# Kernel optimization log

Measured on AMD Instinct MI355X. Metric: run time of the kernel, lower is better.

The kernel has to match this reference:

```python
import jax, jax.numpy as jnp
import numpy as np
from jax import lax

KSIZE = 3
SIGMA = 0.3 * ((KSIZE - 1) * 0.5 - 1) + 0.8  # cv2 auto-sigma for k=3 -> 0.8

def _gauss_kernel(k, sigma):
    ax = np.arange(k, dtype=np.float64) - (k - 1) / 2
    xx, yy = np.meshgrid(ax, ax, indexing='ij')
    ker = np.exp(-(xx ** 2 + yy ** 2) / (2.0 * sigma ** 2))
    ker /= ker.sum()
    return jnp.asarray(ker, jnp.float32)

SCHARR_X = jnp.array([[-3., 0., 3.], [-10., 0., 10.], [-3., 0., 3.]], jnp.float32)
SCHARR_Y = SCHARR_X.T  # cv2.Scharr(dy=1)

def _conv2d_reflect(img, ker):
    # img: [B,1,H,W]; cross-correlation (like cv2.filter2D) with BORDER_REFLECT_101
    p = ker.shape[0] // 2
    img = jnp.pad(img, ((0, 0), (0, 0), (p, p), (p, p)), mode='reflect')
    return lax.conv_general_dilated(img, ker[None, None], (1, 1), 'VALID')

def setup_inputs() -> dict:
    key = jax.random.key(0)
    x = jax.random.uniform(key, (8, 3, 1024, 1024), dtype=jnp.float32) * 255.0
    return {"x": x}

def reference(x):
    B, C, H, W = x.shape
    # cv2 RGB2GRAY weights
    rgb_w = jnp.array([0.299, 0.587, 0.114], dtype=x.dtype)
    gray = jnp.einsum('bchw,c->bhw', x, rgb_w)[:, None]  # [B,1,H,W]
    blurred = _conv2d_reflect(gray, _gauss_kernel(KSIZE, SIGMA))
    sx = _conv2d_reflect(blurred, SCHARR_X)
    sy = _conv2d_reflect(blurred, SCHARR_Y)
    mag = jnp.sqrt(sx * sx + sy * sy)  # L2_gradient=True
    # forward returns gradient magnitude replicated across channels
    return jnp.broadcast_to(mag, (B, C, H, W))
```

## Files before the change

kernel.cpp:

```cpp
#include <hip/hip_runtime.h>
#include <math.h>


#define IMG_H 1024
#define IMG_W 1024
#define TH 32
#define TW 128
#define GYR (TH + 4)
#define GXD 136
#define NIT ((GYR * (GXD/4) + 255) / 256)
#define NITEMS (GYR * (GXD/4))

#define W0 0.52201125f
#define W1 0.23899437f
#define AV0 0.71698311f
#define AV1 3.95597745f
#define AV2 6.65407872f

__device__ __forceinline__ int reflect101(int v, int n) {
    v = (v < 0) ? -v : v;
    return (v >= n) ? (2 * n - 2 - v) : v;
}

__global__ __launch_bounds__(256)
void edge_kernel(const float* __restrict__ in, float* __restrict__ out, int B) {
    __shared__ float sg[GYR][GXD];

    const int tid = threadIdx.x;
    const int x0 = blockIdx.x * TW;
    const int y0 = blockIdx.y * TH;
    const int b  = blockIdx.z;

    const size_t plane = (size_t)IMG_H * IMG_W;
    const float* pr = in + (size_t)b * 3 * plane;
    const float* pg = pr + plane;
    const float* pb = pg + plane;

    float4 R[NIT], G[NIT], Bv[NIT];
    #pragma unroll
    for (int it = 0; it < NIT; ++it) {
        int i = tid + it * 256;
        if (i < NITEMS) {
            int gy  = i / (GXD / 4);
            int gx4 = (i - gy * (GXD / 4)) * 4;
            int y = reflect101(y0 - 2 + gy, IMG_H);
            int x = x0 - 4 + gx4;
            if ((unsigned)x <= (unsigned)(IMG_W - 4)) {
                size_t o = (size_t)y * IMG_W + x;
                R[it]  = *(const float4*)(pr + o);
                G[it]  = *(const float4*)(pg + o);
                Bv[it] = *(const float4*)(pb + o);
            } else {
                int xe0 = reflect101(x,     IMG_W), xe1 = reflect101(x + 1, IMG_W);
                int xe2 = reflect101(x + 2, IMG_W), xe3 = reflect101(x + 3, IMG_W);
                size_t ro = (size_t)y * IMG_W;
                R[it]  = make_float4(pr[ro+xe0], pr[ro+xe1], pr[ro+xe2], pr[ro+xe3]);
                G[it]  = make_float4(pg[ro+xe0], pg[ro+xe1], pg[ro+xe2], pg[ro+xe3]);
                Bv[it] = make_float4(pb[ro+xe0], pb[ro+xe1], pb[ro+xe2], pb[ro+xe3]);
            }
        }
    }
    #pragma unroll
    for (int it = 0; it < NIT; ++it) {
        int i = tid + it * 256;
        if (i < NITEMS) {
            int gy  = i / (GXD / 4);
            int gx4 = (i - gy * (GXD / 4)) * 4;
            float4 gr;
            gr.x = 0.299f * R[it].x + 0.587f * G[it].x + 0.114f * Bv[it].x;
            gr.y = 0.299f * R[it].y + 0.587f * G[it].y + 0.114f * Bv[it].y;
            gr.z = 0.299f * R[it].z + 0.587f * G[it].z + 0.114f * Bv[it].z;
            gr.w = 0.299f * R[it].w + 0.587f * G[it].w + 0.114f * Bv[it].w;
            *(float4*)&sg[gy][gx4] = gr;
        }
    }
    __syncthreads();

    const int tx  = tid & 31;
    const int tyg = tid >> 5;
    const int c4  = tx * 4;
    const int r0  = tyg * 4;

    float hs[5][4], hd[5][4];

    auto hrow = [&](int rr, float* HS, float* HD) {
        const float* row = &sg[rr][c4];
        float4 ga = *(const float4*)(row);
        float4 gb = *(const float4*)(row + 4);
        float4 gc = *(const float4*)(row + 8);
        float g[12] = {ga.x, ga.y, ga.z, ga.w, gb.x, gb.y, gb.z, gb.w,
                       gc.x, gc.y, gc.z, gc.w};
        #pragma unroll
        for (int k = 0; k < 4; ++k) {
            HS[k] = AV0 * (g[k+2] + g[k+6]) + AV1 * (g[k+3] + g[k+5]) + AV2 * g[k+4];
            HD[k] = W1 * (g[k+6] - g[k+2]) + W0 * (g[k+5] - g[k+3]);
        }
    };

    #pragma unroll
    for (int s = 0; s < 5; ++s) hrow(r0 + s, hs[s], hd[s]);

    float* po = out + (size_t)b * 3 * plane;
    #pragma unroll
    for (int t = 0; t < 4; ++t) {
        if (t > 0) hrow(r0 + 4 + t, hs[(t + 4) % 5], hd[(t + 4) % 5]);
        const int i0 = t % 5, i1 = (t+1) % 5, i2 = (t+2) % 5, i3 = (t+3) % 5, i4 = (t+4) % 5;
        float4 mag;
        float* mp = &mag.x;
        #pragma unroll
        for (int k = 0; k < 4; ++k) {
            float sx = AV0 * (hd[i0][k] + hd[i4][k]) + AV1 * (hd[i1][k] + hd[i3][k]) + AV2 * hd[i2][k];
            float sy = W1 * (hs[i4][k] - hs[i0][k]) + W0 * (hs[i3][k] - hs[i1][k]);
            mp[k] = sqrtf(sx * sx + sy * sy);
        }
        size_t o = (size_t)(y0 + r0 + t) * IMG_W + (x0 + c4);
        *(float4*)(po + o)             = mag;
        *(float4*)(po + o + plane)     = mag;
        *(float4*)(po + o + 2 * plane) = mag;
    }
}

extern "C" void kernel_launch(void* const* d_in, const int* in_sizes, int n_in,
                              void* d_out, int out_size, void* d_ws, size_t ws_size,
                              hipStream_t stream) {
    const float* in = (const float*)d_in[0];
    float* out = (float*)d_out;
    const int B = in_sizes[0] / (3 * IMG_H * IMG_W);
    dim3 grid(IMG_W / TW, IMG_H / TH, B);
    edge_kernel<<<grid, dim3(256), 0, stream>>>(in, out, B);
}
```

Before: 178.4 us.

## Shrink tiles to 8 rows, use 1D grid with image-interleaved block order

```diff
diff --git a/kernel.cpp b/kernel.cpp
--- a/kernel.cpp
+++ b/kernel.cpp
@@ -4,15 +4,14 @@
 
 #define IMG_H 1024
 #define IMG_W 1024
-#define TH 32
 #define TW 128
+#define TH 8
 #define GYR (TH + 4)
 #define GXD 136
-#define NIT ((GYR * (GXD/4) + 255) / 256)
-#define NITEMS (GYR * (GXD/4))
+#define NITEMS (GYR * (GXD / 4))
 
-#define W0 0.52201125f
-#define W1 0.23899437f
+#define W0f 0.52201125f
+#define W1f 0.23899437f
 #define AV0 0.71698311f
 #define AV1 3.95597745f
 #define AV2 6.65407872f
@@ -22,102 +21,89 @@
     return (v >= n) ? (2 * n - 2 - v) : v;
 }
 
-__global__ __launch_bounds__(256)
+__global__ __launch_bounds__(256, 8)
 void edge_kernel(const float* __restrict__ in, float* __restrict__ out, int B) {
     __shared__ float sg[GYR][GXD];
 
     const int tid = threadIdx.x;
-    const int x0 = blockIdx.x * TW;
-    const int y0 = blockIdx.y * TH;
-    const int b  = blockIdx.z;
+    const int id  = blockIdx.x;
+
+    int img, slot;
+    if (B == 8) { img = id & 7; slot = id >> 3; }
+    else        { img = id >> 10; slot = id & 1023; }
+    const int y_t = slot & 127;
+    const int x_t = slot >> 7;
+
+    const int x0 = x_t * TW;
+    const int y0 = y_t * TH;
 
     const size_t plane = (size_t)IMG_H * IMG_W;
-    const float* pr = in + (size_t)b * 3 * plane;
-    const float* pg = pr + plane;
-    const float* pb = pg + plane;
+    const float* pr  = in + (size_t)img * 3 * plane;
+    const float* pg  = pr + plane;
+    const float* pbl = pg + plane;
+    float* po = out + (size_t)img * 3 * plane;
 
-    float4 R[NIT], G[NIT], Bv[NIT];
-    #pragma unroll
-    for (int it = 0; it < NIT; ++it) {
-        int i = tid + it * 256;
-        if (i < NITEMS) {
-            int gy  = i / (GXD / 4);
-            int gx4 = (i - gy * (GXD / 4)) * 4;
-            int y = reflect101(y0 - 2 + gy, IMG_H);
-            int x = x0 - 4 + gx4;
-            if ((unsigned)x <= (unsigned)(IMG_W - 4)) {
-                size_t o = (size_t)y * IMG_W + x;
-                R[it]  = *(const float4*)(pr + o);
-                G[it]  = *(const float4*)(pg + o);
-                Bv[it] = *(const float4*)(pb + o);
-            } else {
-                int xe0 = reflect101(x,     IMG_W), xe1 = reflect101(x + 1, IMG_W);
-                int xe2 = reflect101(x + 2, IMG_W), xe3 = reflect101(x + 3, IMG_W);
-                size_t ro = (size_t)y * IMG_W;
-                R[it]  = make_float4(pr[ro+xe0], pr[ro+xe1], pr[ro+xe2], pr[ro+xe3]);
-                G[it]  = make_float4(pg[ro+xe0], pg[ro+xe1], pg[ro+xe2], pg[ro+xe3]);
-                Bv[it] = make_float4(pb[ro+xe0], pb[ro+xe1], pb[ro+xe2], pb[ro+xe3]);
-            }
+    for (int i = tid; i < NITEMS; i += 256) {
+        int gy  = i / (GXD / 4);
+        int gx4 = (i - gy * (GXD / 4)) * 4;
+        int y = reflect101(y0 - 2 + gy, IMG_H);
+        int x = x0 - 4 + gx4;
+        float4 r4, g4, b4;
+        if ((unsigned)x <= (unsigned)(IMG_W - 4)) {
+            size_t o = ((size_t)y << 10) + x;
+            r4 = *(const float4*)(pr  + o);
+            g4 = *(const float4*)(pg  + o);
+            b4 = *(const float4*)(pbl + o);
+        } else {
+            int x0e = reflect101(x,     IMG_W), x1e = reflect101(x + 1, IMG_W);
+            int x2e = reflect101(x + 2, IMG_W), x3e = reflect101(x + 3, IMG_W);
+            size_t ro = (size_t)y << 10;
+            r4 = make_float4(pr[ro+x0e],  pr[ro+x1e],  pr[ro+x2e],  pr[ro+x3e]);
+            g4 = make_float4(pg[ro+x0e],  pg[ro+x1e],  pg[ro+x2e],  pg[ro+x3e]);
+            b4 = make_float4(pbl[ro+x0e], pbl[ro+x1e], pbl[ro+x2e], pbl[ro+x3e]);
         }
-    }
-    #pragma unroll
-    for (int it = 0; it < NIT; ++it) {
-        int i = tid + it * 256;
-        if (i < NITEMS) {
-            int gy  = i / (GXD / 4);
-            int gx4 = (i - gy * (GXD / 4)) * 4;
-            float4 gr;
-            gr.x = 0.299f * R[it].x + 0.587f * G[it].x + 0.114f * Bv[it].x;
-            gr.y = 0.299f * R[it].y + 0.587f * G[it].y + 0.114f * Bv[it].y;
-            gr.z = 0.299f * R[it].z + 0.587f * G[it].z + 0.114f * Bv[it].z;
-            gr.w = 0.299f * R[it].w + 0.587f * G[it].w + 0.114f * Bv[it].w;
-            *(float4*)&sg[gy][gx4] = gr;
-        }
+        float4 gr;
+        gr.x = 0.299f * r4.x + 0.587f * g4.x + 0.114f * b4.x;
+        gr.y = 0.299f * r4.y + 0.587f * g4.y + 0.114f * b4.y;
+        gr.z = 0.299f * r4.z + 0.587f * g4.z + 0.114f * b4.z;
+        gr.w = 0.299f * r4.w + 0.587f * g4.w + 0.114f * b4.w;
+        *(float4*)&sg[gy][gx4] = gr;
     }
     __syncthreads();
 
-    const int tx  = tid & 31;
-    const int tyg = tid >> 5;
-    const int c4  = tx * 4;
-    const int r0  = tyg * 4;
+    const int tx = tid & 31;
+    const int ty = tid >> 5;
+    const int c4 = tx * 4;
 
-    float hs[5][4], hd[5][4];
+    float vs[8] = {}, vd[8] = {};
+    #pragma unroll
+    for (int r = 0; r < 5; ++r) {
+        const float av = (r == 0 || r == 4) ? AV0 : ((r == 1 || r == 3) ? AV1 : AV2);
+        const float dv = (r == 0) ? -W1f : (r == 1) ? -W0f : (r == 3) ? W0f : W1f;
+        float4 va = *(const float4*)&sg[ty + r][c4];
+        float4 vb = *(const float4*)&sg[ty + r][c4 + 4];
+        float4 vc = *(const float4*)&sg[ty + r][c4 + 8];
+        const float g[8] = {va.z, va.w, vb.x, vb.y, vb.z, vb.w, vc.x, vc.y};
+        #pragma unroll
+        for (int j = 0; j < 8; ++j) {
+            vs[j] += av * g[j];
+            if (r != 2) vd[j] += dv * g[j];
+        }
+    }
 
-    auto hrow = [&](int rr, float* HS, float* HD) {
-        const float* row = &sg[rr][c4];
-        float4 ga = *(const float4*)(row);
-        float4 gb = *(const float4*)(row + 4);
-        float4 gc = *(const float4*)(row + 8);
-        float g[12] = {ga.x, ga.y, ga.z, ga.w, gb.x, gb.y, gb.z, gb.w,
-                       gc.x, gc.y, gc.z, gc.w};
-        #pragma unroll
-        for (int k = 0; k < 4; ++k) {
-            HS[k] = AV0 * (g[k+2] + g[k+6]) + AV1 * (g[k+3] + g[k+5]) + AV2 * g[k+4];
-            HD[k] = W1 * (g[k+6] - g[k+2]) + W0 * (g[k+5] - g[k+3]);
-        }
-    };
+    float4 m;
+    float* mp = &m.x;
+    #pragma unroll
+    for (int k = 0; k < 4; ++k) {
+        float sx = W1f * (vs[k+4] - vs[k]) + W0f * (vs[k+3] - vs[k+1]);
+        float sy = AV0 * (vd[k] + vd[k+4]) + AV1 * (vd[k+1] + vd[k+3]) + AV2 * vd[k+2];
+        mp[k] = sqrtf(sx * sx + sy * sy);
+    }
 
-    #pragma unroll
-    for (int s = 0; s < 5; ++s) hrow(r0 + s, hs[s], hd[s]);
-
-    float* po = out + (size_t)b * 3 * plane;
-    #pragma unroll
-    for (int t = 0; t < 4; ++t) {
-        if (t > 0) hrow(r0 + 4 + t, hs[(t + 4) % 5], hd[(t + 4) % 5]);
-        const int i0 = t % 5, i1 = (t+1) % 5, i2 = (t+2) % 5, i3 = (t+3) % 5, i4 = (t+4) % 5;
-        float4 mag;
-        float* mp = &mag.x;
-        #pragma unroll
-        for (int k = 0; k < 4; ++k) {
-            float sx = AV0 * (hd[i0][k] + hd[i4][k]) + AV1 * (hd[i1][k] + hd[i3][k]) + AV2 * hd[i2][k];
-            float sy = W1 * (hs[i4][k] - hs[i0][k]) + W0 * (hs[i3][k] - hs[i1][k]);
-            mp[k] = sqrtf(sx * sx + sy * sy);
-        }
-        size_t o = (size_t)(y0 + r0 + t) * IMG_W + (x0 + c4);
-        *(float4*)(po + o)             = mag;
-        *(float4*)(po + o + plane)     = mag;
-        *(float4*)(po + o + 2 * plane) = mag;
-    }
+    const size_t o = ((size_t)(y0 + ty) << 10) + (x0 + c4);
+    *(float4*)(po + o)             = m;
+    *(float4*)(po + o + plane)     = m;
+    *(float4*)(po + o + 2 * plane) = m;
 }
 
 extern "C" void kernel_launch(void* const* d_in, const int* in_sizes, int n_in,
@@ -126,6 +112,6 @@
     const float* in = (const float*)d_in[0];
     float* out = (float*)d_out;
     const int B = in_sizes[0] / (3 * IMG_H * IMG_W);
-    dim3 grid(IMG_W / TW, IMG_H / TH, B);
-    edge_kernel<<<grid, dim3(256), 0, stream>>>(in, out, B);
+    const int nblocks = B * (IMG_W / TW) * (IMG_H / TH);
+    edge_kernel<<<dim3(nblocks), dim3(256), 0, stream>>>(in, out, B);
 }
```

Result: slower. 200.2 us (+12.3%).
